# Kernel tuning notes

Hardware: AMD Instinct MI355X
Metric: run time of the kernel (lower is better)

Reference implementation:

```python
import jax, jax.numpy as jnp
import numpy as np

B, S, D, H = 2, 2048, 1024, 16
HD = D // H  # 64
ROPE_BASE = 10000.0


def setup_inputs() -> dict:
    key = jax.random.key(0)
    k1, k2, k3 = jax.random.split(key, 3)
    std = 1.0 / np.sqrt(D)
    x = jax.random.normal(k1, (B, S, D), dtype=jnp.float32)
    w_in = jax.random.normal(k2, (3 * D, D), dtype=jnp.float32) * std
    w_out = jax.random.normal(k3, (D, D), dtype=jnp.float32) * (std / np.sqrt(2.0))
    return {"x": x, "w_in": w_in, "w_out": w_out}


def _rope_cos_sin(seq_len, head_dim):
    inv_freq = 1.0 / (ROPE_BASE ** (jnp.arange(0, head_dim, 2, dtype=jnp.float32) / head_dim))
    t = jnp.arange(seq_len, dtype=jnp.float32)
    freqs = jnp.einsum("s,d->sd", t, inv_freq)          # [S, HD/2]
    emb = jnp.concatenate([freqs, freqs], axis=-1)       # [S, HD]
    return jnp.cos(emb)[None, :, None, :], jnp.sin(emb)[None, :, None, :]


def _rotate_half(x):
    x1, x2 = jnp.split(x, 2, axis=-1)
    return jnp.concatenate([-x2, x1], axis=-1)


def _apply_rope(x, cos, sin):
    return x * cos + _rotate_half(x) * sin


def reference(x, w_in, w_out):
    b, s, d = x.shape
    # fused QKV projection (no bias)
    qkv = x @ w_in.T                                      # [B, S, 3D]
    q, k, v = jnp.split(qkv, 3, axis=-1)
    q = q.reshape(b, s, H, HD)
    k = k.reshape(b, s, H, HD)
    v = v.reshape(b, s, H, HD)
    # rotary (offset = 0, no KV cache)
    cos, sin = _rope_cos_sin(s, HD)
    q = _apply_rope(q, cos, sin)
    k = _apply_rope(k, cos, sin)
    # causal SDPA, scale 1/sqrt(head_dim)
    scale = 1.0 / jnp.sqrt(jnp.asarray(HD, dtype=x.dtype))
    scores = jnp.einsum("bqhd,bkhd->bhqk", q, k) * scale  # [B, H, S, S]
    causal = jnp.tril(jnp.ones((s, s), dtype=bool))
    scores = jnp.where(causal, scores, jnp.asarray(-jnp.inf, dtype=scores.dtype))
    attn = jax.nn.softmax(scores, axis=-1)
    out = jnp.einsum("bhqk,bkhd->bqhd", attn, v).reshape(b, s, d)
    return out @ w_out.T
```

## Files before the change

### kernel.cpp

```cpp
#include <hip/hip_runtime.h>
#include <hip/hip_bf16.h>
#include <math.h>

#define NB 2
#define NS 2048
#define ND 1024
#define NH 16
#define HD 64
#define BS (NB*NS)
#define D3 (3*ND)
#define NT (NS/64)

typedef __bf16 bf16;
typedef __bf16 bf16x4 __attribute__((ext_vector_type(4)));
typedef __bf16 bf16x8 __attribute__((ext_vector_type(8)));
typedef float f32x4 __attribute__((ext_vector_type(4)));

#define MFMA16(a,b,c) __builtin_amdgcn_mfma_f32_16x16x32_bf16(a,b,c,0,0,0)

static __device__ inline f32x4 zero4() { f32x4 z; z[0]=0.f; z[1]=0.f; z[2]=0.f; z[3]=0.f; return z; }

__device__ __forceinline__ void gload_lds16(const bf16* g, bf16* l) {
    __builtin_amdgcn_global_load_lds(
        (__attribute__((address_space(1))) unsigned int*)g,
        (__attribute__((address_space(3))) unsigned int*)l, 16, 0, 0);
}

#define CVT1 (BS*ND/8)
#define CVT2 (D3*ND/8)
#define CVT3 (ND*ND/8)
#define CVTN (CVT1+CVT2+CVT3)
__global__ __launch_bounds__(256) void prep(
    const float* __restrict__ x, const float* __restrict__ w_in, const float* __restrict__ w_out,
    bf16* __restrict__ xb, bf16* __restrict__ winb, bf16* __restrict__ woutb,
    float2* __restrict__ csT)
{
    int i = blockIdx.x * 256 + threadIdx.x;
    if (i < CVTN) {
        const float* in; bf16* out; int j;
        if (i < CVT1)            { in = x;     out = xb;    j = i; }
        else if (i < CVT1+CVT2)  { in = w_in;  out = winb;  j = i - CVT1; }
        else                     { in = w_out; out = woutb; j = i - CVT1 - CVT2; }
        const float4* p = (const float4*)in;
        float4 a = p[j*2], b = p[j*2+1];
        bf16x8 o;
        o[0]=(bf16)a.x; o[1]=(bf16)a.y; o[2]=(bf16)a.z; o[3]=(bf16)a.w;
        o[4]=(bf16)b.x; o[5]=(bf16)b.y; o[6]=(bf16)b.z; o[7]=(bf16)b.w;
        ((bf16x8*)out)[j] = o;
    } else {
        int k = i - CVTN;
        int s = k >> 5, j = k & 31;
        float inv = __expf(-(float)j * (9.210340372f * 0.03125f));
        float ang = (float)s * inv;
        csT[k] = make_float2(cosf(ang), sinf(ang));
    }
}

__global__ __launch_bounds__(512, 2) void gemm8_qkv(
    const bf16* __restrict__ A, const bf16* __restrict__ Bm,
    bf16* __restrict__ Qb, bf16* __restrict__ Kb, bf16* __restrict__ Vt,
    const float2* __restrict__ csT)
{
    __shared__ bf16 As[2][256*64];
    __shared__ bf16 Bs[2][256*64];
    int t = threadIdx.x;
    int lane = t & 63, w = t >> 6;
    int wr = w >> 2, wc = w & 3;
    int lr = lane & 15, lg = lane >> 4;
    int m0 = blockIdx.y * 256, n0 = blockIdx.x * 256;

    int srow8 = lane >> 3;
    int schunk = (lane & 7) ^ srow8;
    const bf16* gA = A  + (size_t)(m0 + srow8)*ND + schunk*8;
    const bf16* gB = Bm + (size_t)(n0 + srow8)*ND + schunk*8;

    auto stageA = [&](int kt) {
        int buf = kt & 1, k0 = kt*64;
        #pragma unroll
        for (int i=0;i<2;i++) {
            int r0 = (w*2+i)*8;
            gload_lds16(gA + (size_t)r0*ND + k0,       &As[buf][r0*64]);
            gload_lds16(gA + (size_t)(128+r0)*ND + k0, &As[buf][(128+r0)*64]);
        }
    };
    auto stageB = [&](int kt) {
        int buf = kt & 1, k0 = kt*64;
        #pragma unroll
        for (int i=0;i<2;i++) {
            int r0 = (w*2+i)*8;
            gload_lds16(gB + (size_t)r0*ND + k0,       &Bs[buf][r0*64]);
            gload_lds16(gB + (size_t)(128+r0)*ND + k0, &Bs[buf][(128+r0)*64]);
        }
    };

    f32x4 acc[8][4];
    #pragma unroll
    for (int m=0;m<8;m++)
        #pragma unroll
        for (int n=0;n<4;n++) acc[m][n] = zero4();

    bf16x8 af[4][2], bfr[4][2];

    stageB(0); stageA(0); stageB(1); stageA(1);

    for (int kt = 0; kt < 16; kt++) {
        int cur = kt & 1;
        const bf16* as = &As[cur][0];
        const bf16* bs = &Bs[cur][0];
        if (kt < 15) asm volatile("s_waitcnt vmcnt(8)" ::: "memory");
        else         asm volatile("s_waitcnt vmcnt(0)" ::: "memory");
        __builtin_amdgcn_s_barrier();
        __builtin_amdgcn_sched_barrier(0);

        #pragma unroll
        for (int m=0;m<4;m++) {
            int row = wr*128 + m*16 + lr;
            af[m][0] = *(const bf16x8*)&as[row*64 + ((lg     ^ (row&7))*8)];
            af[m][1] = *(const bf16x8*)&as[row*64 + (((4+lg) ^ (row&7))*8)];
        }
        #pragma unroll
        for (int n=0;n<2;n++) {
            int row = wc*64 + n*16 + lr;
            bfr[n][0] = *(const bf16x8*)&bs[row*64 + ((lg     ^ (row&7))*8)];
            bfr[n][1] = *(const bf16x8*)&bs[row*64 + (((4+lg) ^ (row&7))*8)];
        }
        asm volatile("s_waitcnt lgkmcnt(0)" ::: "memory");
        __builtin_amdgcn_sched_barrier(0);
        __builtin_amdgcn_s_setprio(1);
        #pragma unroll
        for (int ks=0;ks<2;ks++)
            #pragma unroll
            for (int m=0;m<4;m++)
                #pragma unroll
                for (int n=0;n<2;n++)
                    acc[m][n] = MFMA16(af[m][ks], bfr[n][ks], acc[m][n]);
        __builtin_amdgcn_s_setprio(0);
        __builtin_amdgcn_s_barrier();
        __builtin_amdgcn_sched_barrier(0);

        #pragma unroll
        for (int n=2;n<4;n++) {
            int row = wc*64 + n*16 + lr;
            bfr[n][0] = *(const bf16x8*)&bs[row*64 + ((lg     ^ (row&7))*8)];
            bfr[n][1] = *(const bf16x8*)&bs[row*64 + (((4+lg) ^ (row&7))*8)];
        }
        asm volatile("s_waitcnt lgkmcnt(0)" ::: "memory");
        __builtin_amdgcn_sched_barrier(0);
        __builtin_amdgcn_s_setprio(1);
        #pragma unroll
        for (int ks=0;ks<2;ks++)
            #pragma unroll
            for (int m=0;m<4;m++)
                #pragma unroll
                for (int n=2;n<4;n++)
                    acc[m][n] = MFMA16(af[m][ks], bfr[n][ks], acc[m][n]);
        __builtin_amdgcn_s_setprio(0);
        __builtin_amdgcn_s_barrier();
        __builtin_amdgcn_sched_barrier(0);

        if (kt + 2 < 16) stageB(kt + 2);
        #pragma unroll
        for (int m=0;m<4;m++) {
            int row = wr*128 + (m+4)*16 + lr;
            af[m][0] = *(const bf16x8*)&as[row*64 + ((lg     ^ (row&7))*8)];
            af[m][1] = *(const bf16x8*)&as[row*64 + (((4+lg) ^ (row&7))*8)];
        }
        asm volatile("s_waitcnt lgkmcnt(0)" ::: "memory");
        __builtin_amdgcn_sched_barrier(0);
        __builtin_amdgcn_s_setprio(1);
        #pragma unroll
        for (int ks=0;ks<2;ks++)
            #pragma unroll
            for (int m=0;m<4;m++)
                #pragma unroll
                for (int n=0;n<2;n++)
                    acc[m+4][n] = MFMA16(af[m][ks], bfr[n][ks], acc[m+4][n]);
        __builtin_amdgcn_s_setprio(0);
        __builtin_amdgcn_s_barrier();
        __builtin_amdgcn_sched_barrier(0);

        if (kt + 2 < 16) stageA(kt + 2);
        __builtin_amdgcn_s_setprio(1);
        #pragma unroll
        for (int ks=0;ks<2;ks++)
            #pragma unroll
            for (int m=0;m<4;m++)
                #pragma unroll
                for (int n=2;n<4;n++)
                    acc[m+4][n] = MFMA16(af[m][ks], bfr[n][ks], acc[m+4][n]);
        __builtin_amdgcn_s_setprio(0);
    }

    int which = n0 >> 10;
    if (which == 2) {
        #pragma unroll
        for (int m=0;m<8;m++)
            #pragma unroll
            for (int n=0;n<4;n++) {
                int grow = m0 + wr*128 + m*16 + lg*4;
                int gcol = n0 + wc*64 + n*16 + lr;
                int h = (gcol & 1023) >> 6, d = gcol & 63;
                int b = grow >> 11, s0 = grow & (NS-1);
                int shi = s0 & ~63, j = s0 & 63;
                int kp = ((j>>5)&1)*32 + ((j>>2)&3)*8 + ((j>>4)&1)*4;
                bf16x4 pv;
                #pragma unroll
                for (int r=0;r<4;r++) pv[r] = (bf16)acc[m][n][r];
                *(bf16x4*)&Vt[((size_t)((b*NH + h)*HD + d))*NS + shi + kp] = pv;
            }
    } else {
        const float qs = 0.125f * 1.44269504f;
        bf16* dst = (which == 0) ? Qb : Kb;
        #pragma unroll
        for (int m=0;m<8;m++) {
            int grow = m0 + wr*128 + m*16 + lg*4;
            #pragma unroll
            for (int n=0;n<2;n++) {
                int gcol = n0 + wc*64 + n*16 + lr;
                int h = (gcol & 1023) >> 6, j = gcol & 63;
                #pragma unroll
                for (int r=0;r<4;r++) {
                    int gm = grow + r;
                    int b = gm >> 11, s = gm & (NS-1);
                    float2 cs = csT[(s<<5)+j];
                    float x1 = acc[m][n][r], x2 = acc[m][n+2][r];
                    float y1 = x1*cs.x - x2*cs.y;
                    float y2 = x2*cs.x + x1*cs.y;
                    if (which == 0) { y1 *= qs; y2 *= qs; }
                    size_t off = ((size_t)((b*NH + h)*NS + s))*HD;
                    dst[off + j]      = (bf16)y1;
                    dst[off + j + 32] = (bf16)y2;
                }
            }
        }
    }
}

__global__ __launch_bounds__(256) void gemm_out(
    const bf16* __restrict__ A, const bf16* __restrict__ Bm,
    float* __restrict__ C, int M, int N, int K)
{
    __shared__ bf16 As[2][128*64];
    __shared__ bf16 Bs[2][128*64];
    int t = threadIdx.x;
    int lane = t & 63, w = t >> 6;
    int wr = w >> 1, wc = w & 1;
    int lr = lane & 15, lg = lane >> 4;
    int m0 = blockIdx.y * 128, n0 = blockIdx.x * 128;

    int srow = lane >> 3;
    int schunk = (lane & 7) ^ srow;
    const bf16* gA = &A [(size_t)(m0 + w*32 + srow)*K + schunk*8];
    const bf16* gB = &Bm[(size_t)(n0 + w*32 + srow)*K + schunk*8];

    auto stage = [&](int kt) {
        int buf = kt & 1;
        bf16* lA = &As[buf][w*2048];
        bf16* lB = &Bs[buf][w*2048];
        int k0 = kt * 64;
        #pragma unroll
        for (int i=0;i<4;i++) {
            gload_lds16(gA + (size_t)(i*8)*K + k0, lA + i*512);
            gload_lds16(gB + (size_t)(i*8)*K + k0, lB + i*512);
        }
    };

    f32x4 acc[4][4];
    for (int m=0;m<4;m++) for (int n=0;n<4;n++) acc[m][n] = zero4();

    int nt = K >> 6;
    stage(0);
    stage(1);

    for (int kt = 0; kt < nt; kt++) {
        int cur = kt & 1;
        if (kt < nt-1) asm volatile("s_waitcnt vmcnt(8)" ::: "memory");
        else           asm volatile("s_waitcnt vmcnt(0)" ::: "memory");
        __builtin_amdgcn_s_barrier();
        __builtin_amdgcn_sched_barrier(0);

        bf16x8 af[2][4], bfr[2][4];
        #pragma unroll
        for (int ks=0;ks<2;ks++) {
            #pragma unroll
            for (int m=0;m<4;m++) {
                int row = wr*64 + m*16 + lr;
                af[ks][m] = *(const bf16x8*)&As[cur][row*64 + (((ks*4+lg) ^ (row&7))*8)];
            }
            #pragma unroll
            for (int n=0;n<4;n++) {
                int row = wc*64 + n*16 + lr;
                bfr[ks][n] = *(const bf16x8*)&Bs[cur][row*64 + (((ks*4+lg) ^ (row&7))*8)];
            }
        }
        asm volatile("s_waitcnt lgkmcnt(0)" ::: "memory");
        __builtin_amdgcn_sched_barrier(0);
        __builtin_amdgcn_s_barrier();
        __builtin_amdgcn_sched_barrier(0);

        if (kt + 2 < nt) stage(kt + 2);

        __builtin_amdgcn_s_setprio(1);
        #pragma unroll
        for (int ks=0;ks<2;ks++)
            #pragma unroll
            for (int m=0;m<4;m++)
                #pragma unroll
                for (int n=0;n<4;n++)
                    acc[m][n] = MFMA16(af[ks][m], bfr[ks][n], acc[m][n]);
        __builtin_amdgcn_s_setprio(0);
    }

    for (int m=0;m<4;m++) for (int n=0;n<4;n++) {
        int grow = m0 + wr*64 + m*16 + lg*4;
        int gcol = n0 + wc*64 + n*16 + lr;
        for (int r=0;r<4;r++)
            C[(size_t)(grow+r) * N + gcol] = acc[m][n][r];
    }
}

__global__ __launch_bounds__(256, 4) void attn_fwd(
    const bf16* __restrict__ Qb, const bf16* __restrict__ Kb, const bf16* __restrict__ Vp,
    bf16* __restrict__ AO)
{
    __shared__ bf16 Ks[2][64*64];
    __shared__ bf16 Vs[2][64*64];
    int t = threadIdx.x;
    int lane = t & 63, w = t >> 6;
    int lr = lane & 15, lg = lane >> 4;
    int wgid = blockIdx.x;
    int g = wgid >> 5;
    int qt = (g < 8) ? 31 - g : (g < 16) ? g - 8 : (g < 24) ? 39 - g : g - 16;
    int bh = wgid & 31;
    int b = bh >> 4, h = bh & 15;
    size_t base = (size_t)bh * NS * HD;
    int q0 = qt*64 + w*16;

    bf16x8 qf[2];
    #pragma unroll
    for (int c=0;c<2;c++)
        qf[c] = *(const bf16x8*)&Qb[base + (size_t)(q0+lr)*HD + c*32 + lg*8];

    bf16x8 onesf;
    #pragma unroll
    for (int i=0;i<8;i++) onesf[i] = (bf16)1.0f;

    f32x4 o[4];
    f32x4 lacc = zero4();
    #pragma unroll
    for (int n=0;n<4;n++) o[n] = zero4();
    f32x4 minit;
    minit[0] = -12.f; minit[1] = -12.f; minit[2] = -12.f; minit[3] = -12.f;

    int srow8 = lane >> 3;
    int schunk = (lane & 7) ^ srow8;
    int srcrow = w*8 + srow8;
    const bf16* gK = Kb + base + (size_t)srcrow*HD + schunk*8;
    const bf16* gV = Vp + base + (size_t)srcrow*NS + schunk*8;

    auto stage = [&](int kt) {
        int buf = kt & 1;
        int kv0 = kt * 64;
        #pragma unroll
        for (int i=0;i<2;i++) {
            gload_lds16(gK + (size_t)(kv0 + i*32)*HD, &Ks[buf][(i*32 + w*8)*64]);
            gload_lds16(gV + (size_t)(i*32)*NS + kv0, &Vs[buf][(i*32 + w*8)*64]);
        }
    };

    stage(0);
    if (qt > 0) stage(1);

    for (int kt = 0; kt <= qt; kt++) {
        int cur = kt & 1;
        bool last = (kt == qt);
        if (!last) asm volatile("s_waitcnt vmcnt(4)" ::: "memory");
        else       asm volatile("s_waitcnt vmcnt(0)" ::: "memory");
        __builtin_amdgcn_s_barrier();
        __builtin_amdgcn_sched_barrier(0);

        const bf16* ksb = &Ks[cur][0];
        const bf16* vsb = &Vs[cur][0];

        bf16x8 kf[4][2], vf[2][4];
        #pragma unroll
        for (int kb=0;kb<4;kb++) {
            int row = kb*16 + lr;
            kf[kb][0] = *(const bf16x8*)&ksb[row*64 + ((lg     ^ (row&7))*8)];
            kf[kb][1] = *(const bf16x8*)&ksb[row*64 + (((4+lg) ^ (row&7))*8)];
        }
        #pragma unroll
        for (int c=0;c<2;c++)
            #pragma unroll
            for (int n=0;n<4;n++) {
                int row = n*16 + lr;
                vf[c][n] = *(const bf16x8*)&vsb[row*64 + (((c*4+lg) ^ (row&7))*8)];
            }

        f32x4 sc[4];
        __builtin_amdgcn_s_setprio(1);
        #pragma unroll
        for (int kb=0;kb<4;kb++) {
            sc[kb] = MFMA16(kf[kb][0], qf[0], minit);
            sc[kb] = MFMA16(kf[kb][1], qf[1], sc[kb]);
        }
        __builtin_amdgcn_s_setprio(0);

        if (last) {
            int qi = q0 + lr;
            #pragma unroll
            for (int kb=0;kb<4;kb++)
                #pragma unroll
                for (int rr=0;rr<4;rr++)
                    if (kt*64 + kb*16 + lg*4 + rr > qi) sc[kb][rr] = -__builtin_inff();
        }

        bf16x8 pa[2];
        #pragma unroll
        for (int c=0;c<2;c++) {
            bf16x8 v;
            #pragma unroll
            for (int i=0;i<8;i++) v[i] = (bf16)exp2f(sc[c*2 + (i>>2)][i&3]);
            pa[c] = v;
        }

        asm volatile("s_waitcnt lgkmcnt(0)" ::: "memory");
        __builtin_amdgcn_sched_barrier(0);
        __builtin_amdgcn_s_barrier();
        __builtin_amdgcn_sched_barrier(0);

        if (kt + 2 <= qt) stage(kt + 2);

        __builtin_amdgcn_s_setprio(1);
        #pragma unroll
        for (int c=0;c<2;c++) {
            lacc = MFMA16(onesf, pa[c], lacc);
            #pragma unroll
            for (int n=0;n<4;n++)
                o[n] = MFMA16(vf[c][n], pa[c], o[n]);
        }
        __builtin_amdgcn_s_setprio(0);
    }

    float inv = 1.0f / lacc[0];
    int q = q0 + lr;
    #pragma unroll
    for (int n=0;n<4;n++) {
        bf16x4 ov;
        #pragma unroll
        for (int rr=0;rr<4;rr++) ov[rr] = (bf16)(o[n][rr] * inv);
        *(bf16x4*)&AO[((size_t)(b*NS + q)*NH + h)*HD + n*16 + lg*4] = ov;
    }
}

extern "C" void kernel_launch(void* const* d_in, const int* in_sizes, int n_in,
                              void* d_out, int out_size, void* d_ws, size_t ws_size,
                              hipStream_t stream) {
    const float* x     = (const float*)d_in[0];
    const float* w_in  = (const float*)d_in[1];
    const float* w_out = (const float*)d_in[2];
    float* out = (float*)d_out;

    char* p = (char*)d_ws;
    bf16* xb    = (bf16*)p; p += (size_t)BS*ND*2;
    bf16* winb  = (bf16*)p; p += (size_t)D3*ND*2;
    bf16* woutb = (bf16*)p; p += (size_t)ND*ND*2;
    bf16* Qb    = (bf16*)p; p += (size_t)NB*NH*NS*HD*2;
    bf16* Kb    = (bf16*)p; p += (size_t)NB*NH*NS*HD*2;
    bf16* Vp    = (bf16*)p; p += (size_t)NB*NH*NS*HD*2;
    bf16* AO    = (bf16*)p; p += (size_t)BS*ND*2;
    float2* csT = (float2*)p; p += (size_t)NS*32*8;

    prep<<<(CVTN + NS*32)/256, 256, 0, stream>>>(x, w_in, w_out, xb, winb, woutb, csT);
    gemm8_qkv<<<dim3(D3/256, BS/256), 512, 0, stream>>>(xb, winb, Qb, Kb, Vp, csT);
    attn_fwd<<<NB*NH*NT, 256, 0, stream>>>(Qb, Kb, Vp, AO);
    gemm_out<<<dim3(ND/128, BS/128), 256, 0, stream>>>(AO, woutb, out, BS, ND, ND);
}
```

Before: 95.95 us.

## Load K/V fragments directly from global memory, dropping LDS staging

```diff
diff --git a/kernel.cpp b/kernel.cpp
--- a/kernel.cpp
+++ b/kernel.cpp
@@ -323,8 +323,6 @@
     const bf16* __restrict__ Qb, const bf16* __restrict__ Kb, const bf16* __restrict__ Vp,
     bf16* __restrict__ AO)
 {
-    __shared__ bf16 Ks[2][64*64];
-    __shared__ bf16 Vs[2][64*64];
     int t = threadIdx.x;
     int lane = t & 63, w = t >> 6;
     int lr = lane & 15, lg = lane >> 4;
@@ -352,50 +350,24 @@
     f32x4 minit;
     minit[0] = -12.f; minit[1] = -12.f; minit[2] = -12.f; minit[3] = -12.f;
 
-    int srow8 = lane >> 3;
-    int schunk = (lane & 7) ^ srow8;
-    int srcrow = w*8 + srow8;
-    const bf16* gK = Kb + base + (size_t)srcrow*HD + schunk*8;
-    const bf16* gV = Vp + base + (size_t)srcrow*NS + schunk*8;
-
-    auto stage = [&](int kt) {
-        int buf = kt & 1;
-        int kv0 = kt * 64;
-        #pragma unroll
-        for (int i=0;i<2;i++) {
-            gload_lds16(gK + (size_t)(kv0 + i*32)*HD, &Ks[buf][(i*32 + w*8)*64]);
-            gload_lds16(gV + (size_t)(i*32)*NS + kv0, &Vs[buf][(i*32 + w*8)*64]);
-        }
-    };
-
-    stage(0);
-    if (qt > 0) stage(1);
+    const bf16* kbase = Kb + base + (size_t)lr*HD + lg*8;
+    const bf16* vbase = Vp + base + (size_t)lr*NS + lg*8;
 
     for (int kt = 0; kt <= qt; kt++) {
-        int cur = kt & 1;
+        int kv0 = kt*64;
         bool last = (kt == qt);
-        if (!last) asm volatile("s_waitcnt vmcnt(4)" ::: "memory");
-        else       asm volatile("s_waitcnt vmcnt(0)" ::: "memory");
-        __builtin_amdgcn_s_barrier();
-        __builtin_amdgcn_sched_barrier(0);
-
-        const bf16* ksb = &Ks[cur][0];
-        const bf16* vsb = &Vs[cur][0];
 
         bf16x8 kf[4][2], vf[2][4];
         #pragma unroll
-        for (int kb=0;kb<4;kb++) {
-            int row = kb*16 + lr;
-            kf[kb][0] = *(const bf16x8*)&ksb[row*64 + ((lg     ^ (row&7))*8)];
-            kf[kb][1] = *(const bf16x8*)&ksb[row*64 + (((4+lg) ^ (row&7))*8)];
-        }
+        for (int kb=0;kb<4;kb++)
+            #pragma unroll
+            for (int c=0;c<2;c++)
+                kf[kb][c] = *(const bf16x8*)&kbase[(size_t)(kv0 + kb*16)*HD + c*32];
         #pragma unroll
         for (int c=0;c<2;c++)
             #pragma unroll
-            for (int n=0;n<4;n++) {
-                int row = n*16 + lr;
-                vf[c][n] = *(const bf16x8*)&vsb[row*64 + (((c*4+lg) ^ (row&7))*8)];
-            }
+            for (int n=0;n<4;n++)
+                vf[c][n] = *(const bf16x8*)&vbase[(size_t)(n*16)*NS + kv0 + c*32];
 
         f32x4 sc[4];
         __builtin_amdgcn_s_setprio(1);
@@ -412,7 +384,7 @@
             for (int kb=0;kb<4;kb++)
                 #pragma unroll
                 for (int rr=0;rr<4;rr++)
-                    if (kt*64 + kb*16 + lg*4 + rr > qi) sc[kb][rr] = -__builtin_inff();
+                    if (kv0 + kb*16 + lg*4 + rr > qi) sc[kb][rr] = -__builtin_inff();
         }
 
         bf16x8 pa[2];
@@ -423,13 +395,6 @@
             for (int i=0;i<8;i++) v[i] = (bf16)exp2f(sc[c*2 + (i>>2)][i&3]);
             pa[c] = v;
         }
-
-        asm volatile("s_waitcnt lgkmcnt(0)" ::: "memory");
-        __builtin_amdgcn_sched_barrier(0);
-        __builtin_amdgcn_s_barrier();
-        __builtin_amdgcn_sched_barrier(0);
-
-        if (kt + 2 <= qt) stage(kt + 2);
 
         __builtin_amdgcn_s_setprio(1);
         #pragma unroll
```

Result: slower. 183.6 us (+91.4%).
